# Kernel tuning notes

Measured on AMD Instinct MI355X. Metric: run time of the kernel, lower is better.

## Reference

```python
import jax, jax.numpy as jnp
import numpy as np

LEAKY_SLOPE = 0.01  # torch nn.LeakyReLU default

def leaky_relu(x):
    return jnp.where(x >= 0, x, LEAKY_SLOPE * x)

def setup_inputs() -> dict:
    key = jax.random.key(0)
    ks = jax.random.split(key, 11)
    B, F, C_IN, H, K, D = 2048, 512, 3, 64, 8, 128  # batch, features, expand, layer_conf[0], bucket_num, bucket_dim
    ASR, MM, OUT = 128, 768, 256
    proj_in = ASR + MM + F * D
    inp = {
        "stat_features": jax.random.uniform(ks[0], (B, F), dtype=jnp.float32),
        "asr_embeddings": jax.random.normal(ks[1], (B, ASR), dtype=jnp.float32),
        "mm_embeddings": jax.random.normal(ks[2], (B, MM), dtype=jnp.float32),
        "linear1_w": jax.random.normal(ks[3], (F, C_IN, H), dtype=jnp.float32) * (1.0 / np.sqrt(C_IN)),
        "linear1_b": jax.random.normal(ks[4], (F, 1, H), dtype=jnp.float32),
        "linear2_w": jax.random.normal(ks[5], (F, H, K), dtype=jnp.float32) * (1.0 / np.sqrt(H)),
        "linear2_b": jax.random.normal(ks[6], (F, 1, K), dtype=jnp.float32),
        "tau": jnp.ones((F, 1, K), dtype=jnp.float32),
        "emb": jax.random.normal(ks[7], (F, K, D), dtype=jnp.float32),
        "proj_w": jax.random.normal(ks[8], (OUT, proj_in), dtype=jnp.float32) * (1.0 / np.sqrt(proj_in)),
        "proj_b": jax.random.normal(ks[9], (OUT,), dtype=jnp.float32) * 0.01,
    }
    return inp

def reference(stat_features, asr_embeddings, mm_embeddings,
              linear1_w, linear1_b, linear2_w, linear2_b, tau, emb,
              proj_w, proj_b):
    # sanitize: NaN -> 0, negatives -> 0
    x = stat_features
    x = jnp.where(jnp.isnan(x) | (x < 0.0), 0.0, x)  # [B, F]

    # auto_dis: per-feature tiny MLP. x is expanded to 3 identical copies -> [B,F,1,3]
    # matmul with [F,3,H] == einsum over the 3 copies.
    B, F = x.shape
    x3 = jnp.broadcast_to(x[:, :, None], (B, F, 3))           # [B,F,3]
    h = jnp.einsum('bfc,fch->bfh', x3, linear1_w) + linear1_b[:, 0, :]  # [B,F,H]
    h = jnp.where(h >= 0, h, LEAKY_SLOPE * h)
    s = jnp.einsum('bfh,fhk->bfk', h, linear2_w) + linear2_b[:, 0, :]   # [B,F,K]
    s = jnp.where(s >= 0, s, LEAKY_SLOPE * s)
    s = s * tau[:, 0, :]
    p = jax.nn.softmax(s, axis=-1)                            # [B,F,K]
    y = jnp.einsum('bfk,fkd->bfd', p, emb)                    # [B,F,D]
    y = y.reshape(B, -1)                                      # [B, F*D] (fc = Identity)

    z = jnp.concatenate([asr_embeddings, mm_embeddings, y], axis=1)
    out = jax.nn.relu(z @ proj_w.T + proj_b)                  # [B, 256]
    return out
```

## Files before the change

### kernel.cpp

```cpp
#include <hip/hip_runtime.h>
#include <hip/hip_bf16.h>
#include <math.h>

#define LEAKY 0.01f
#define B_    2048
#define F_    512
#define H_    64
#define K_    8
#define D_    128
#define ASR_  128
#define MM_   768
#define OUT_  256
#define PROJ_IN 66432
#define ZK    4992
#define NSPLIT 8


typedef unsigned short u16;
typedef u16   u16x8 __attribute__((ext_vector_type(8)));
typedef short s16x8 __attribute__((ext_vector_type(8)));
typedef float f32x4 __attribute__((ext_vector_type(4)));

__device__ __forceinline__ u16 f2bf(float x) {
  unsigned int u = __float_as_uint(x);
  u += 0x7fffu + ((u >> 16) & 1u);
  return (u16)(u >> 16);
}

__device__ __forceinline__ float quad_sum(float g) {
  int a = __builtin_amdgcn_update_dpp(0, __float_as_int(g), 0xB1, 0xF, 0xF, true);
  g += __int_as_float(a);
  int b = __builtin_amdgcn_update_dpp(0, __float_as_int(g), 0x4E, 0xF, 0xF, true);
  return g + __int_as_float(b);
}

__device__ __forceinline__ void ldrow(float4 (&b)[8], const float* p) {
  #pragma unroll
  for (int j = 0; j < 8; ++j) b[j] = *(const float4*)(p + j * 4);
}

__device__ __forceinline__ float dot32(const float4 (&b)[8], const float4 (&e)[8]) {
  float gp0 = 0.f, gp1 = 0.f;
  #pragma unroll
  for (int j = 0; j < 8; ++j) {
    gp0 = fmaf(e[j].x, b[j].x, gp0);
    gp1 = fmaf(e[j].y, b[j].y, gp1);
    gp0 = fmaf(e[j].z, b[j].z, gp0);
    gp1 = fmaf(e[j].w, b[j].w, gp1);
  }
  return gp0 + gp1;
}

#define PRODUCER_BLOCKS (512 + 1024 + 896 + 224)

__global__ __launch_bounds__(256) void producer_kernel(
    const float* __restrict__ stat, const float* __restrict__ w1,
    const float* __restrict__ b1v, const float* __restrict__ w2,
    const float* __restrict__ b2v, const float* __restrict__ tauv,
    const float* __restrict__ pw, const float* __restrict__ emb,
    const float* __restrict__ asr, const float* __restrict__ mm,
    u16* __restrict__ A0, u16* __restrict__ Pf, u16* __restrict__ Wn) {
  __shared__ __align__(16) char smem[15616];
  const int bid = blockIdx.x;
  const int t = threadIdx.x;

  if (bid < 512) {
    const int f0 = (bid >> 3) * 8;
    const int o0 = (bid & 7) * 32;
    const int fl = t >> 5, k = (t >> 2) & 7, dq = t & 3;
    float4 e[8];
    {
      const float* ep = emb + ((size_t)(f0 + fl) * 8 + k) * 128 + dq * 32;
      #pragma unroll
      for (int j = 0; j < 8; ++j) e[j] = *(const float4*)(ep + j * 4);
    }
    const float* gsrc = pw + 896 + (size_t)(f0 + fl) * 128 + dq * 32
                        + (size_t)o0 * PROJ_IN;
    u16* wdst = Wn + 896 + (size_t)(f0 + fl) * 8 + k;
    float4 bufA[8], bufB[8];
    ldrow(bufA, gsrc);
    #pragma unroll
    for (int rr2 = 0; rr2 < 16; ++rr2) {
      const int r0 = 2 * rr2;
      ldrow(bufB, gsrc + (size_t)(r0 + 1) * PROJ_IN);
      {
        float g = quad_sum(dot32(bufA, e));
        if (dq == 0) wdst[(size_t)(o0 + r0) * ZK] = f2bf(g);
      }
      if (r0 + 2 < 32)
        ldrow(bufA, gsrc + (size_t)(r0 + 2) * PROJ_IN);
      {
        float g = quad_sum(dot32(bufB, e));
        if (dq == 0) wdst[(size_t)(o0 + r0 + 1) * ZK] = f2bf(g);
      }
    }
  } else if (bid < 1536) {
    const int pb = bid - 512;
    const int f0 = (pb & 127) * 4;
    const int b0 = (pb >> 7) * 256;
    float* s_w1s = (float*)(smem);
    float* s_b1  = (float*)(smem + 1024);
    float* s_x   = (float*)(smem + 2048);
    {
      int fl = t >> 6, h = t & 63;
      const float* wf = w1 + (size_t)(f0 + fl) * 192;
      s_w1s[fl * 64 + h] = wf[h] + wf[64 + h] + wf[128 + h];
      s_b1[fl * 64 + h] = b1v[(size_t)(f0 + fl) * 64 + h];
    }
    {
      float4 sv = *(const float4*)(stat + (size_t)(b0 + t) * F_ + f0);
      float* xr_ = s_x + t * 5;
      xr_[0] = (sv.x >= 0.f) ? sv.x : 0.f;
      xr_[1] = (sv.y >= 0.f) ? sv.y : 0.f;
      xr_[2] = (sv.z >= 0.f) ? sv.z : 0.f;
      xr_[3] = (sv.w >= 0.f) ? sv.w : 0.f;
    }
    __syncthreads();

    const int w = t >> 6;
    const int wu = __builtin_amdgcn_readfirstlane(w);
    const int lane = t & 63;
    const float* w1p = s_w1s + w * 64;
    const float* b1p = s_b1 + w * 64;
    const float* w2u  = w2   + (size_t)(f0 + wu) * 512;
    const float* b2u  = b2v  + (size_t)(f0 + wu) * 8;
    const float* tauu = tauv + (size_t)(f0 + wu) * 8;
    float x[4];
    #pragma unroll
    for (int p = 0; p < 4; ++p) x[p] = s_x[(lane + 64 * p) * 5 + w];
    float acc[4][8] = {{0.f}};
    #pragma unroll 4
    for (int i = 0; i < 64; ++i) {
      float wv = w1p[i], bv = b1p[i];
      float4 wa = *(const float4*)(w2u + i * 8);
      float4 wb = *(const float4*)(w2u + i * 8 + 4);
      #pragma unroll
      for (int p = 0; p < 4; ++p) {
        float h0 = fmaf(x[p], wv, bv);
        float h = fmaf(LEAKY, fminf(h0, 0.f), fmaxf(h0, 0.f));
        acc[p][0] = fmaf(h, wa.x, acc[p][0]);
        acc[p][1] = fmaf(h, wa.y, acc[p][1]);
        acc[p][2] = fmaf(h, wa.z, acc[p][2]);
        acc[p][3] = fmaf(h, wa.w, acc[p][3]);
        acc[p][4] = fmaf(h, wb.x, acc[p][4]);
        acc[p][5] = fmaf(h, wb.y, acc[p][5]);
        acc[p][6] = fmaf(h, wb.z, acc[p][6]);
        acc[p][7] = fmaf(h, wb.w, acc[p][7]);
      }
    }
    #pragma unroll
    for (int p = 0; p < 4; ++p) {
      float s[K_];
      float m = -1e30f;
      #pragma unroll
      for (int kk = 0; kk < K_; ++kk) {
        float v = acc[p][kk] + b2u[kk];
        v = (v >= 0.f) ? v : LEAKY * v;
        v *= tauu[kk];
        s[kk] = v;
        m = fmaxf(m, v);
      }
      float sum = 0.f;
      #pragma unroll
      for (int kk = 0; kk < K_; ++kk) { s[kk] = __expf(s[kk] - m); sum += s[kk]; }
      float inv = 1.f / sum;
      u16x8 hv;
      #pragma unroll
      for (int kk = 0; kk < K_; ++kk) hv[kk] = f2bf(s[kk] * inv);
      *(u16x8*)(Pf + ((size_t)(f0 + w) * B_ + b0 + lane + 64 * p) * 8) = hv;
    }
  } else if (bid < 2432) {
    const int item = bid - 1536;
    const int cidx = item * 256 + t;
    const int r = cidx / 112, c = cidx % 112;
    float4 v0, v1;
    if (c < 16) {
      const float* s = asr + (size_t)r * ASR_ + c * 8;
      v0 = *(const float4*)(s); v1 = *(const float4*)(s + 4);
    } else {
      const float* s = mm + (size_t)r * MM_ + (c - 16) * 8;
      v0 = *(const float4*)(s); v1 = *(const float4*)(s + 4);
    }
    u16x8 hv = {f2bf(v0.x), f2bf(v0.y), f2bf(v0.z), f2bf(v0.w),
                f2bf(v1.x), f2bf(v1.y), f2bf(v1.z), f2bf(v1.w)};
    *(u16x8*)(A0 + (size_t)r * 896 + c * 8) = hv;
  } else {
    const int item = bid - 2432;
    #pragma unroll
    for (int rr = 0; rr < 4; ++rr) {
      int idx = item * 1024 + rr * 256 + t;
      int o = idx / 896, j = idx % 896;
      Wn[(size_t)o * ZK + j] = f2bf(pw[(size_t)o * PROJ_IN + j]);
    }
  }
}

#define SAS 72
__global__ __launch_bounds__(256) void gemm_kernel(
    const u16* __restrict__ A0, const u16* __restrict__ Pf,
    const u16* __restrict__ Wn, float* __restrict__ part) {
  const int bm0 = blockIdx.x * 64;
  const int bn0 = blockIdx.y * 64;
  const int kz  = blockIdx.z;
  const int it0 = kz * 10;
  const int itn = (kz == 7) ? 8 : 10;
  __shared__ u16 sA[64 * SAS];
  __shared__ u16 sB[64 * SAS];
  const int t = threadIdx.x;
  const int w = t >> 6, L = t & 63;
  const int l16 = L & 15, q8 = (L >> 4) * 8;
  const int wm = (w >> 1) * 32, wn = (w & 1) * 32;
  const int row = t >> 2, lk = t & 3;
  const int pp = t >> 5, pg = t & 31;
  f32x4 acc[2][2] = {{{0.f,0.f,0.f,0.f},{0.f,0.f,0.f,0.f}},
                     {{0.f,0.f,0.f,0.f},{0.f,0.f,0.f,0.f}}};
  u16x8 ra[2], rb[2];

#define LOAD_TILES(IT)                                                        \
  {                                                                           \
    const int k0_ = (IT) * 64;                                                \
    if (k0_ < 896) {                                                          \
      const u16* s_ = A0 + (size_t)(bm0 + row) * 896 + k0_ + lk * 8;          \
      ra[0] = *(const u16x8*)(s_);                                            \
      ra[1] = *(const u16x8*)(s_ + 32);                                       \
    } else {                                                                  \
      const int fb_ = (k0_ - 896) >> 3;                                       \
      const u16* s_ = Pf + ((size_t)(fb_ + pp) * B_ + bm0 + pg) * 8;          \
      ra[0] = *(const u16x8*)(s_);                                            \
      ra[1] = *(const u16x8*)(s_ + 256);                        \
    }                                                                         \
    const u16* sb_ = Wn + (size_t)(bn0 + row) * ZK + k0_ + lk * 8;            \
    rb[0] = *(const u16x8*)(sb_);                                             \
    rb[1] = *(const u16x8*)(sb_ + 32);                                        \
  }

#define STORE_TILES(IT)                                                       \
  {                                                                           \
    if ((IT) * 64 < 896) {                                                    \
      *(u16x8*)&sA[row * SAS + lk * 8]      = ra[0];                          \
      *(u16x8*)&sA[row * SAS + lk * 8 + 32] = ra[1];                          \
    } else {                                                                  \
      *(u16x8*)&sA[pg * SAS + pp * 8]        = ra[0];                         \
      *(u16x8*)&sA[(pg + 32) * SAS + pp * 8] = ra[1];                         \
    }                                                                         \
    *(u16x8*)&sB[row * SAS + lk * 8]      = rb[0];                            \
    *(u16x8*)&sB[row * SAS + lk * 8 + 32] = rb[1];                            \
  }

  LOAD_TILES(it0);
  for (int it = it0; it < it0 + itn; ++it) {
    __syncthreads();
    STORE_TILES(it);
    __syncthreads();
    if (it + 1 < it0 + itn) LOAD_TILES(it + 1);
    #pragma unroll
    for (int ks = 0; ks < 2; ++ks) {
      s16x8 a0 = *(const s16x8*)&sA[(wm + l16) * SAS + ks * 32 + q8];
      s16x8 a1 = *(const s16x8*)&sA[(wm + 16 + l16) * SAS + ks * 32 + q8];
      s16x8 b0 = *(const s16x8*)&sB[(wn + l16) * SAS + ks * 32 + q8];
      s16x8 b1 = *(const s16x8*)&sB[(wn + 16 + l16) * SAS + ks * 32 + q8];
      acc[0][0] = __builtin_amdgcn_mfma_f32_16x16x32_bf16(a0, b0, acc[0][0], 0, 0, 0);
      acc[0][1] = __builtin_amdgcn_mfma_f32_16x16x32_bf16(a0, b1, acc[0][1], 0, 0, 0);
      acc[1][0] = __builtin_amdgcn_mfma_f32_16x16x32_bf16(a1, b0, acc[1][0], 0, 0, 0);
      acc[1][1] = __builtin_amdgcn_mfma_f32_16x16x32_bf16(a1, b1, acc[1][1], 0, 0, 0);
    }
  }
#undef LOAD_TILES
#undef STORE_TILES

  float* dst = part + (size_t)kz * B_ * OUT_;
  #pragma unroll
  for (int mf = 0; mf < 2; ++mf) {
    const int r0 = bm0 + wm + mf * 16 + (L >> 4) * 4;
    #pragma unroll
    for (int nf = 0; nf < 2; ++nf) {
      const int col = bn0 + wn + nf * 16 + l16;
      #pragma unroll
      for (int i = 0; i < 4; ++i)
        dst[(size_t)(r0 + i) * OUT_ + col] = acc[mf][nf][i];
    }
  }
}

__global__ __launch_bounds__(256) void combine_kernel(
    const float* __restrict__ part, const float* __restrict__ pb,
    float* __restrict__ out) {
  const int idx4 = (blockIdx.x * 256 + threadIdx.x) * 4;
  const int o = idx4 & (OUT_ - 1);
  float4 bv = *(const float4*)(pb + o);
  float4 r = bv;
  #pragma unroll
  for (int kz = 0; kz < NSPLIT; ++kz) {
    float4 a = *(const float4*)(part + (size_t)kz * B_ * OUT_ + idx4);
    r.x += a.x; r.y += a.y; r.z += a.z; r.w += a.w;
  }
  r.x = r.x > 0.f ? r.x : 0.f;
  r.y = r.y > 0.f ? r.y : 0.f;
  r.z = r.z > 0.f ? r.z : 0.f;
  r.w = r.w > 0.f ? r.w : 0.f;
  *(float4*)(out + idx4) = r;
}

extern "C" void kernel_launch(void* const* d_in, const int* in_sizes, int n_in,
                              void* d_out, int out_size, void* d_ws, size_t ws_size,
                              hipStream_t stream) {
  (void)in_sizes; (void)n_in; (void)out_size; (void)ws_size;
  const float* stat = (const float*)d_in[0];
  const float* asr  = (const float*)d_in[1];
  const float* mm   = (const float*)d_in[2];
  const float* w1   = (const float*)d_in[3];
  const float* b1   = (const float*)d_in[4];
  const float* w2   = (const float*)d_in[5];
  const float* b2   = (const float*)d_in[6];
  const float* tau  = (const float*)d_in[7];
  const float* emb  = (const float*)d_in[8];
  const float* pw   = (const float*)d_in[9];
  const float* pb   = (const float*)d_in[10];
  float* out = (float*)d_out;
  char* ws = (char*)d_ws;
  u16*   A0   = (u16*)(ws);
  u16*   Pf   = (u16*)(ws + 3670016);
  u16*   Wn   = (u16*)(ws + 20447232);
  float* part = (float*)(ws + 23003136);

  producer_kernel<<<PRODUCER_BLOCKS, 256, 0, stream>>>(
      stat, w1, b1, w2, b2, tau, pw, emb, asr, mm, A0, Pf, Wn);
  gemm_kernel<<<dim3(B_ / 64, OUT_ / 64, NSPLIT), 256, 0, stream>>>(
      A0, Pf, Wn, part);
  combine_kernel<<<B_ * OUT_ / 1024, 256, 0, stream>>>(part, pb, out);
}
```

Before: 188.2 us.

## Stage proj weight rows through swizzled LDS for coalesced folding; halve split-K

The embedding-folding part of the producer now has each wave load a proj_w row once with coalesced float4 loads. The row goes into a per-wave, XOR-swizzled LDS buffer, and each lane reads its 32-float slice back from there. Before, each lane did 8 strided float4 global loads, and the eight k-lanes of a feature re-read the same addresses. Separately, the GEMM split-K factor drops from 8 to 4, so each block covers 20 k-iterations and there are fewer partial sums to reduce. The risks are that LDS round trips add latency, the wave-local reuse of the buffer depends on lockstep execution with no barrier, and the GEMM grid has fewer blocks.

```diff
diff --git a/kernel.cpp b/kernel.cpp
--- a/kernel.cpp
+++ b/kernel.cpp
@@ -13,7 +13,7 @@
 #define OUT_  256
 #define PROJ_IN 66432
 #define ZK    4992
-#define NSPLIT 8
+#define NSPLIT 4
 
 
 typedef unsigned short u16;
@@ -32,23 +32,6 @@
   g += __int_as_float(a);
   int b = __builtin_amdgcn_update_dpp(0, __float_as_int(g), 0x4E, 0xF, 0xF, true);
   return g + __int_as_float(b);
-}
-
-__device__ __forceinline__ void ldrow(float4 (&b)[8], const float* p) {
-  #pragma unroll
-  for (int j = 0; j < 8; ++j) b[j] = *(const float4*)(p + j * 4);
-}
-
-__device__ __forceinline__ float dot32(const float4 (&b)[8], const float4 (&e)[8]) {
-  float gp0 = 0.f, gp1 = 0.f;
-  #pragma unroll
-  for (int j = 0; j < 8; ++j) {
-    gp0 = fmaf(e[j].x, b[j].x, gp0);
-    gp1 = fmaf(e[j].y, b[j].y, gp1);
-    gp0 = fmaf(e[j].z, b[j].z, gp0);
-    gp1 = fmaf(e[j].w, b[j].w, gp1);
-  }
-  return gp0 + gp1;
 }
 
 #define PRODUCER_BLOCKS (512 + 1024 + 896 + 224)
@@ -67,31 +50,58 @@
   if (bid < 512) {
     const int f0 = (bid >> 3) * 8;
     const int o0 = (bid & 7) * 32;
-    const int fl = t >> 5, k = (t >> 2) & 7, dq = t & 3;
+    const int w = t >> 6, lam = t & 63;
+    const int fl = lam >> 5, k = (lam >> 2) & 7, dq = lam & 3;
+    const int fbase = f0 + 2 * w;
+    float* sw = (float*)smem + w * 512;
+    float* buf0 = sw;
+    float* buf1 = sw + 256;
+    const int wslot = lam ^ ((lam >> 3) & 7);
+    const int xr = fl * 4 + dq;
     float4 e[8];
     {
-      const float* ep = emb + ((size_t)(f0 + fl) * 8 + k) * 128 + dq * 32;
+      const float* ep = emb + ((size_t)(fbase + fl) * 8 + k) * 128 + dq * 32;
       #pragma unroll
       for (int j = 0; j < 8; ++j) e[j] = *(const float4*)(ep + j * 4);
     }
-    const float* gsrc = pw + 896 + (size_t)(f0 + fl) * 128 + dq * 32
-                        + (size_t)o0 * PROJ_IN;
-    u16* wdst = Wn + 896 + (size_t)(f0 + fl) * 8 + k;
-    float4 bufA[8], bufB[8];
-    ldrow(bufA, gsrc);
-    #pragma unroll
-    for (int rr2 = 0; rr2 < 16; ++rr2) {
-      const int r0 = 2 * rr2;
-      ldrow(bufB, gsrc + (size_t)(r0 + 1) * PROJ_IN);
+    const float* gsrc = pw + 896 + (size_t)fbase * 128
+                        + (size_t)o0 * PROJ_IN + lam * 4;
+    u16* wdst = Wn + (size_t)o0 * ZK + 896 + (size_t)(fbase + fl) * 8 + k;
+    const float* rd0 = buf0 + fl * 128 + dq * 32;
+    const float* rd1 = buf1 + fl * 128 + dq * 32;
+    float4 va = *(const float4*)(gsrc);
+    for (int rr = 0; rr < 16; ++rr) {
+      const int r = 2 * rr;
+      float4 vb = *(const float4*)(gsrc + (size_t)(r + 1) * PROJ_IN);
+      *(float4*)(buf0 + wslot * 4) = va;
       {
-        float g = quad_sum(dot32(bufA, e));
-        if (dq == 0) wdst[(size_t)(o0 + r0) * ZK] = f2bf(g);
+        float g0 = 0.f, g1 = 0.f;
+        #pragma unroll
+        for (int j = 0; j < 8; ++j) {
+          float4 p4 = *(const float4*)(rd0 + 4 * (j ^ xr));
+          g0 = fmaf(e[j].x, p4.x, g0);
+          g1 = fmaf(e[j].y, p4.y, g1);
+          g0 = fmaf(e[j].z, p4.z, g0);
+          g1 = fmaf(e[j].w, p4.w, g1);
+        }
+        float g = quad_sum(g0 + g1);
+        if (dq == 0) wdst[(size_t)r * ZK] = f2bf(g);
       }
-      if (r0 + 2 < 32)
-        ldrow(bufA, gsrc + (size_t)(r0 + 2) * PROJ_IN);
+      if (r + 2 < 32)
+        va = *(const float4*)(gsrc + (size_t)(r + 2) * PROJ_IN);
+      *(float4*)(buf1 + wslot * 4) = vb;
       {
-        float g = quad_sum(dot32(bufB, e));
-        if (dq == 0) wdst[(size_t)(o0 + r0 + 1) * ZK] = f2bf(g);
+        float g0 = 0.f, g1 = 0.f;
+        #pragma unroll
+        for (int j = 0; j < 8; ++j) {
+          float4 p4 = *(const float4*)(rd1 + 4 * (j ^ xr));
+          g0 = fmaf(e[j].x, p4.x, g0);
+          g1 = fmaf(e[j].y, p4.y, g1);
+          g0 = fmaf(e[j].z, p4.z, g0);
+          g1 = fmaf(e[j].w, p4.w, g1);
+        }
+        float g = quad_sum(g0 + g1);
+        if (dq == 0) wdst[(size_t)(r + 1) * ZK] = f2bf(g);
       }
     }
   } else if (bid < 1536) {
@@ -202,8 +212,8 @@
   const int bm0 = blockIdx.x * 64;
   const int bn0 = blockIdx.y * 64;
   const int kz  = blockIdx.z;
-  const int it0 = kz * 10;
-  const int itn = (kz == 7) ? 8 : 10;
+  const int it0 = kz * 20;
+  const int itn = (kz == 3) ? 18 : 20;
   __shared__ u16 sA[64 * SAS];
   __shared__ u16 sB[64 * SAS];
   const int t = threadIdx.x;
```

New measurement: 157.6 us. -16.3%, faster.
